# Performance work log

Hardware: AMD Instinct MI355X
Metric: run time of the kernel (lower is better)

## Reference

```python
import jax, jax.numpy as jnp
import numpy as np

V, D, NH, NL, HID = 128000, 512, 8, 2, 1408
HD = D // NH
HALF = HD // 2
B, T, NLAB, LBL = 4, 508, 5, 4
EPS = 1e-5


def setup_inputs() -> dict:
    key = jax.random.key(0)
    ks = jax.random.split(key, 16)
    g = lambda k, sh: (jax.random.normal(k, sh, jnp.float32) * 0.02)
    return {
        "input_ids": jax.random.randint(ks[0], (B, T), 0, V),
        "label_ids": jax.random.randint(ks[1], (NLAB, LBL), 0, V),
        "emb": g(ks[2], (V, D)),
        "wq": g(ks[3], (NL, D, D)),
        "wk": g(ks[4], (NL, D, D)),
        "wv": g(ks[5], (NL, D, D)),
        "wo": g(ks[6], (NL, D, D)),
        "w1": g(ks[7], (NL, D, HID)),
        "w2": g(ks[8], (NL, HID, D)),
        "w3": g(ks[9], (NL, D, HID)),
        "attn_norm_w": jnp.ones((NL, D), jnp.float32),
        "ffn_norm_w": jnp.ones((NL, D), jnp.float32),
        "final_norm_w": jnp.ones((D,), jnp.float32),
        "lm_head": g(ks[10], (D, V)),
    }


def _rmsnorm(x, w):
    return x * jax.lax.rsqrt(jnp.mean(x * x, axis=-1, keepdims=True) + EPS) * w


def _score(input_ids, label_ids, emb, wq, wk, wv, wo, w1, w2, w3,
           attn_norm_w, ffn_norm_w, final_norm_w, lm_head):
    Bc, Tc = input_ids.shape
    nl, Lc = label_ids.shape
    S = Tc + Lc
    # pad_id is None in the original (tokenizer attr missing) -> all lengths == T.
    # Causal attention => one forward over [prefix || label] equals the per-token re-forwards.
    ctx = jnp.concatenate([
        jnp.broadcast_to(input_ids[None], (nl, Bc, Tc)),
        jnp.broadcast_to(label_ids[:, None, :], (nl, Bc, Lc)),
    ], axis=-1).reshape(nl * Bc, S)
    N = nl * Bc

    h = emb[ctx]  # [N, S, D]

    # RoPE tables
    pos = jnp.arange(S, dtype=jnp.float32)
    freqs = 1.0 / (10000.0 ** (jnp.arange(HALF, dtype=jnp.float32) / HALF))
    ang = pos[:, None] * freqs[None, :]  # [S, HALF]
    cos = jnp.cos(ang)[None, :, None, :]
    sin = jnp.sin(ang)[None, :, None, :]

    def rope(x):  # x: [N, S, NH, HD]
        x1, x2 = x[..., :HALF], x[..., HALF:]
        return jnp.concatenate([x1 * cos - x2 * sin, x1 * sin + x2 * cos], axis=-1)

    causal = jnp.tril(jnp.ones((S, S), dtype=bool))
    scale = 1.0 / jnp.sqrt(jnp.float32(HD))

    for l in range(NL):
        xn = _rmsnorm(h, attn_norm_w[l])
        q = rope((xn @ wq[l]).reshape(N, S, NH, HD))
        k = rope((xn @ wk[l]).reshape(N, S, NH, HD))
        v = (xn @ wv[l]).reshape(N, S, NH, HD)
        scores = jnp.einsum('nqhd,nkhd->nhqk', q, k) * scale
        scores = jnp.where(causal, scores, jnp.float32(-1e9))
        p = jax.nn.softmax(scores, axis=-1)
        o = jnp.einsum('nhqk,nkhd->nqhd', p, v).reshape(N, S, D)
        h = h + o @ wo[l]
        xn = _rmsnorm(h, ffn_norm_w[l])
        h = h + (jax.nn.silu(xn @ w1[l]) * (xn @ w3[l])) @ w2[l]

    h = _rmsnorm(h, final_norm_w)
    # Only positions T-1 .. T+L-2 predict label tokens; project only those.
    hs = h[:, Tc - 1:Tc - 1 + Lc, :]                    # [N, L, D]
    lp = jax.nn.log_softmax(hs @ lm_head, axis=-1)      # [N, L, V]
    lp = lp.reshape(nl, Bc, Lc, V)
    idx = jnp.broadcast_to(label_ids[:, None, :, None], (nl, Bc, Lc, 1))
    tok_lp = jnp.take_along_axis(lp, idx, axis=-1)[..., 0]  # [nl, B, L]
    return tok_lp.sum(axis=-1).T.astype(jnp.float32)        # [B, num_labels]


def reference(input_ids, label_ids, emb, wq, wk, wv, wo, w1, w2, w3,
              attn_norm_w, ffn_norm_w, final_norm_w, lm_head):
    return _score(input_ids, label_ids, emb, wq, wk, wv, wo, w1, w2, w3,
                  attn_norm_w, ffn_norm_w, final_norm_w, lm_head)
```

## Files before the change

kernel.cpp:

```cpp
#include <hip/hip_runtime.h>
#include <math.h>

typedef unsigned short u16;
typedef unsigned int u32;

namespace {
constexpr int kV = 128000, kD = 512, kNH = 8, kNL = 2, kHID = 1408;
constexpr int kHD = 64, kB = 4, kT = 508, kNLAB = 5, kLBL = 4;
constexpr int kS = 512;
constexpr int kNSeq = kNLAB * kB;
constexpr int kNS = kNSeq * kS;
constexpr int kQKV = 1536;
constexpr float kEps = 1e-5f;
constexpr int kNChunk = 2000;
constexpr int kPad = 56;
constexpr int kStr = 72;
constexpr int kPL = 3211264;
constexpr int oWQ = 0, oWK = 262144, oWV = 524288, oWO = 786432;
constexpr int oW1 = 1048576, oW3 = 1769472, oW2 = 2490368;
}

typedef __attribute__((ext_vector_type(8))) short bf16x8;
typedef __attribute__((ext_vector_type(4))) float f32x4;

__device__ inline u32 pk2(float lo, float hi) {
  u32 ul = __builtin_bit_cast(u32, lo);
  u32 uh = __builtin_bit_cast(u32, hi);
  ul += 0x7fffu + ((ul >> 16) & 1u);
  uh += 0x7fffu + ((uh >> 16) & 1u);
  return (ul >> 16) | (uh & 0xffff0000u);
}
__device__ inline u16 bf1(float x) {
  u32 u = __builtin_bit_cast(u32, x);
  u += 0x7fffu + ((u >> 16) & 1u);
  return (u16)(u >> 16);
}
__device__ inline float bf2f(u16 u) {
  return __builtin_bit_cast(float, ((u32)u) << 16);
}
__device__ inline void gload16(const void* g, void* l) {
  __builtin_amdgcn_global_load_lds(
      (const __attribute__((address_space(1))) void*)g,
      (__attribute__((address_space(3))) void*)l, 16, 0, 0);
}

__global__ __launch_bounds__(256) void k_wtrans_all(const float* __restrict__ wq,
                                                    const float* __restrict__ wk,
                                                    const float* __restrict__ wv,
                                                    const float* __restrict__ wo,
                                                    const float* __restrict__ w1,
                                                    const float* __restrict__ w3,
                                                    const float* __restrict__ w2,
                                                    u16* __restrict__ wT) {
  int bid = blockIdx.x;
  int l = bid / 3136, r = bid % 3136;
  const float* src; u16* dst; int K, N, gxw, t; float scale = 1.f;
  if (r < 1024) {
    int w = r >> 8; t = r & 255; K = 512; N = 512; gxw = 16;
    src = (w == 0 ? wq : w == 1 ? wk : w == 2 ? wv : wo) + (size_t)l * 262144;
    dst = wT + (size_t)l * kPL + w * 262144;
    if (w == 0) scale = 0.125f;
  } else if (r < 2432) {
    int rr = r - 1024; int w = rr / 704; t = rr - w * 704; K = 512; N = 1408; gxw = 44;
    src = (w ? w3 : w1) + (size_t)l * 720896;
    dst = wT + (size_t)l * kPL + (w ? oW3 : oW1);
  } else {
    t = r - 2432; K = 1408; N = 512; gxw = 16;
    src = w2 + (size_t)l * 720896;
    dst = wT + (size_t)l * kPL + oW2;
  }
  int bn = (t % gxw) * 32, bk = (t / gxw) * 32;
  __shared__ float tb[32][33];
  int tid = threadIdx.x;
  int rr2 = tid >> 3, c4 = (tid & 7) * 4;
  float4 v = *(const float4*)(src + (size_t)(bk + rr2) * N + bn + c4);
  tb[rr2][c4 + 0] = v.x * scale; tb[rr2][c4 + 1] = v.y * scale;
  tb[rr2][c4 + 2] = v.z * scale; tb[rr2][c4 + 3] = v.w * scale;
  __syncthreads();
  uint2 o;
  o.x = pk2(tb[c4 + 0][rr2], tb[c4 + 1][rr2]);
  o.y = pk2(tb[c4 + 2][rr2], tb[c4 + 3][rr2]);
  *(uint2*)&dst[(size_t)(bn + rr2) * K + bk + c4] = o;
}

__global__ void k_embed(const int* __restrict__ input_ids, const int* __restrict__ label_ids,
                        const float* __restrict__ emb, float* __restrict__ h) {
  int row = blockIdx.x;
  int n = row / kS, s = row - n * kS;
  int lab = n / kB, b = n - lab * kB;
  int tok = (s < kT) ? input_ids[b * kT + s] : label_ids[lab * kLBL + (s - kT)];
  const float4* src = (const float4*)(emb + (size_t)tok * kD);
  float4* dst = (float4*)(h + (size_t)row * kD);
  for (int i = threadIdx.x; i < kD / 4; i += blockDim.x) dst[i] = src[i];
}

__global__ __launch_bounds__(256) void k_rmsnorm(const float* __restrict__ x,
                                                 const float* __restrict__ w,
                                                 u16* __restrict__ y) {
  int row = blockIdx.x;
  int tid = threadIdx.x;
  const float* xr = x + (size_t)row * kD;
  int i = tid * 2;
  float v0 = xr[i], v1 = xr[i + 1];
  float ss = v0 * v0 + v1 * v1;
  #pragma unroll
  for (int o = 1; o < 64; o <<= 1) ss += __shfl_xor(ss, o);
  __shared__ float wsum[4];
  int lane = tid & 63, wid = tid >> 6;
  if (lane == 0) wsum[wid] = ss;
  __syncthreads();
  float tot = wsum[0] + wsum[1] + wsum[2] + wsum[3];
  float inv = rsqrtf(tot / (float)kD + kEps);
  *(u32*)&y[(size_t)row * kD + i] = pk2(v0 * inv * w[i], v1 * inv * w[i + 1]);
}

template<int MODE>
__global__ __launch_bounds__(256) void k_gemm_bf16(const u16* __restrict__ A,
                                                   const u16* __restrict__ Bt,
                                                   void* __restrict__ Cv,
                                                   int M, int N, int K, int gx) {
  __shared__ u16 As[4 * 128 * 16];
  __shared__ u16 Bs[4 * 128 * 16];
  int nwg = gridDim.x;
  int q8 = nwg >> 3;
  int wg = (blockIdx.x & 7) * q8 + (blockIdx.x >> 3);
  int by = wg / gx, bx = wg - by * gx;
  int row0 = by * 128, col0 = bx * 128;
  int tid = threadIdx.x;
  int wave = tid >> 6, lane = tid & 63;
  int wm = wave >> 1, wn = wave & 1;
  int l15 = lane & 15, l16 = lane >> 4;
  f32x4 acc[4][4];
  #pragma unroll
  for (int i = 0; i < 4; i++)
    #pragma unroll
    for (int j = 0; j < 4; j++) acc[i][j] = (f32x4){0.f, 0.f, 0.f, 0.f};

  int sR = lane >> 1, sS = (lane & 1) * 8;

  for (int k0 = 0; k0 < K; k0 += 64) {
    #pragma unroll
    for (int i = 0; i < 4; i++) {
      int rr = i * 32 + sR;
      gload16(A + (size_t)(row0 + rr) * K + k0 + wave * 16 + sS,
              (char*)As + (wave * 4 + i) * 1024);
      gload16(Bt + (size_t)(col0 + rr) * K + k0 + wave * 16 + sS,
              (char*)Bs + (wave * 4 + i) * 1024);
    }
    __syncthreads();
    #pragma unroll
    for (int kk = 0; kk < 2; kk++) {
      int qq = kk * 2 + (l16 >> 1);
      int sub = (l16 & 1) * 8;
      bf16x8 af[4], bfr[4];
      #pragma unroll
      for (int mf = 0; mf < 4; mf++)
        af[mf] = *(const bf16x8*)&As[qq * 2048 + (wm * 64 + mf * 16 + l15) * 16 + sub];
      #pragma unroll
      for (int nf = 0; nf < 4; nf++)
        bfr[nf] = *(const bf16x8*)&Bs[qq * 2048 + (wn * 64 + nf * 16 + l15) * 16 + sub];
      #pragma unroll
      for (int mf = 0; mf < 4; mf++)
        #pragma unroll
        for (int nf = 0; nf < 4; nf++)
          acc[mf][nf] = __builtin_amdgcn_mfma_f32_16x16x32_bf16(af[mf], bfr[nf], acc[mf][nf], 0, 0, 0);
    }
    __syncthreads();
  }
  #pragma unroll
  for (int mf = 0; mf < 4; mf++)
    #pragma unroll
    for (int nf = 0; nf < 4; nf++)
      #pragma unroll
      for (int r = 0; r < 4; r++) {
        int row = row0 + wm * 64 + mf * 16 + l16 * 4 + r;
        int col = col0 + wn * 64 + nf * 16 + l15;
        size_t off = (size_t)row * N + col;
        if (MODE == 1) ((float*)Cv)[off] += acc[mf][nf][r];
        else           ((u16*)Cv)[off] = bf1(acc[mf][nf][r]);
      }
}

__global__ __launch_bounds__(256) void k_ffn13_bf16(const u16* __restrict__ A,
                                                    const u16* __restrict__ W1t,
                                                    const u16* __restrict__ W3t,
                                                    u16* __restrict__ act,
                                                    int M, int N, int K, int gx) {
  __shared__ u16 As[4 * 128 * 16];
  __shared__ u16 B1[4 * 128 * 16];
  __shared__ u16 B2[4 * 128 * 16];
  int nwg = gridDim.x;
  int q8 = nwg >> 3;
  int wg = (blockIdx.x & 7) * q8 + (blockIdx.x >> 3);
  int by = wg / gx, bx = wg - by * gx;
  int row0 = by * 128, col0 = bx * 128;
  int tid = threadIdx.x;
  int wave = tid >> 6, lane = tid & 63;
  int wm = wave >> 1, wn = wave & 1;
  int l15 = lane & 15, l16 = lane >> 4;
  f32x4 acc1[4][4], acc2[4][4];
  #pragma unroll
  for (int i = 0; i < 4; i++)
    #pragma unroll
    for (int j = 0; j < 4; j++) {
      acc1[i][j] = (f32x4){0.f, 0.f, 0.f, 0.f};
      acc2[i][j] = (f32x4){0.f, 0.f, 0.f, 0.f};
    }
  int sR = lane >> 1, sS = (lane & 1) * 8;

  for (int k0 = 0; k0 < K; k0 += 64) {
    #pragma unroll
    for (int i = 0; i < 4; i++) {
      int rr = i * 32 + sR;
      gload16(A   + (size_t)(row0 + rr) * K + k0 + wave * 16 + sS,
              (char*)As + (wave * 4 + i) * 1024);
      gload16(W1t + (size_t)(col0 + rr) * K + k0 + wave * 16 + sS,
              (char*)B1 + (wave * 4 + i) * 1024);
      gload16(W3t + (size_t)(col0 + rr) * K + k0 + wave * 16 + sS,
              (char*)B2 + (wave * 4 + i) * 1024);
    }
    __syncthreads();
    #pragma unroll
    for (int kk = 0; kk < 2; kk++) {
      int qq = kk * 2 + (l16 >> 1);
      int sub = (l16 & 1) * 8;
      bf16x8 af[4], b1f[4], b2f[4];
      #pragma unroll
      for (int mf = 0; mf < 4; mf++)
        af[mf] = *(const bf16x8*)&As[qq * 2048 + (wm * 64 + mf * 16 + l15) * 16 + sub];
      #pragma unroll
      for (int nf = 0; nf < 4; nf++) {
        b1f[nf] = *(const bf16x8*)&B1[qq * 2048 + (wn * 64 + nf * 16 + l15) * 16 + sub];
        b2f[nf] = *(const bf16x8*)&B2[qq * 2048 + (wn * 64 + nf * 16 + l15) * 16 + sub];
      }
      #pragma unroll
      for (int mf = 0; mf < 4; mf++)
        #pragma unroll
        for (int nf = 0; nf < 4; nf++) {
          acc1[mf][nf] = __builtin_amdgcn_mfma_f32_16x16x32_bf16(af[mf], b1f[nf], acc1[mf][nf], 0, 0, 0);
          acc2[mf][nf] = __builtin_amdgcn_mfma_f32_16x16x32_bf16(af[mf], b2f[nf], acc2[mf][nf], 0, 0, 0);
        }
    }
    __syncthreads();
  }
  #pragma unroll
  for (int mf = 0; mf < 4; mf++)
    #pragma unroll
    for (int nf = 0; nf < 4; nf++)
      #pragma unroll
      for (int r = 0; r < 4; r++) {
        int row = row0 + wm * 64 + mf * 16 + l16 * 4 + r;
        int col = col0 + wn * 64 + nf * 16 + l15;
        float aa = acc1[mf][nf][r];
        float sg = 1.f / (1.f + expf(-aa));
        act[(size_t)row * N + col] = bf1(aa * sg * acc2[mf][nf][r]);
      }
}

__global__ void k_rope(u16* __restrict__ qkv) {
  int idx = blockIdx.x * blockDim.x + threadIdx.x;
  if (idx >= kNS * kNH * 16) return;
  int d2 = (idx & 15) * 2;
  int t = idx >> 4;
  int hh = t & (kNH - 1);
  int row = t >> 3;
  int s = row & (kS - 1);
  float fa = expf(-0.2878231366242558f * (float)d2);
  float fb = expf(-0.2878231366242558f * (float)(d2 + 1));
  float aa = (float)s * fa, ab = (float)s * fb;
  float ca = cosf(aa), sa = sinf(aa);
  float cb = cosf(ab), sb = sinf(ab);
  size_t base = (size_t)row * kQKV + hh * kHD + d2;
  u32 q1 = *(u32*)&qkv[base], q2 = *(u32*)&qkv[base + 32];
  float x1a = bf2f((u16)q1), x1b = bf2f((u16)(q1 >> 16));
  float x2a = bf2f((u16)q2), x2b = bf2f((u16)(q2 >> 16));
  *(u32*)&qkv[base]      = pk2(x1a * ca - x2a * sa, x1b * cb - x2b * sb);
  *(u32*)&qkv[base + 32] = pk2(x1a * sa + x2a * ca, x1b * sb + x2b * cb);
  u32 k1 = *(u32*)&qkv[base + 512], k2 = *(u32*)&qkv[base + 544];
  x1a = bf2f((u16)k1); x1b = bf2f((u16)(k1 >> 16));
  x2a = bf2f((u16)k2); x2b = bf2f((u16)(k2 >> 16));
  *(u32*)&qkv[base + 512] = pk2(x1a * ca - x2a * sa, x1b * cb - x2b * sb);
  *(u32*)&qkv[base + 544] = pk2(x1a * sa + x2a * ca, x1b * sb + x2b * cb);
}

__global__ __launch_bounds__(256) void k_attn_mfma(const u16* __restrict__ qkv,
                                                   u16* __restrict__ o) {
  int qt = blockIdx.x;
  int nh = blockIdx.y;
  int hh = nh & (kNH - 1), n = nh >> 3;
  int tid = threadIdx.x;
  int wq = tid >> 6, lane = tid & 63;
  int l15 = lane & 15, l16 = lane >> 4;
  __shared__ u16 Ks[64 * kStr];
  __shared__ u16 Vt[64 * kStr];
  __shared__ u16 Ps[4][16 * kStr];
  int q0 = qt * 64;
  int qrow = q0 + wq * 16 + l15;

  bf16x8 qf[2];
  {
    const u16* qg = qkv + (size_t)(n * kS + qrow) * kQKV + hh * kHD;
    qf[0] = *(const bf16x8*)(qg + l16 * 8);
    qf[1] = *(const bf16x8*)(qg + 32 + l16 * 8);
  }

  f32x4 oacc[4];
  #pragma unroll
  for (int i = 0; i < 4; i++) oacc[i] = (f32x4){0.f, 0.f, 0.f, 0.f};
  float m_run = -1e30f, l_run = 0.f;

  int skv = tid & 63, sd0 = (tid >> 6) * 16;

  for (int jt = 0; jt <= qt; jt++) {
    int j0 = jt * 64;
    __syncthreads();
    {
      size_t gb = (size_t)(n * kS + j0 + skv) * kQKV + 512 + hh * kHD + sd0;
      const u16* kg = qkv + gb;
      *(uint4*)&Ks[skv * kStr + sd0]     = *(const uint4*)kg;
      *(uint4*)&Ks[skv * kStr + sd0 + 8] = *(const uint4*)(kg + 8);
      union { uint4 u4[2]; u16 us[16]; } vb;
      vb.u4[0] = *(const uint4*)(kg + 512);
      vb.u4[1] = *(const uint4*)(kg + 520);
      #pragma unroll
      for (int i = 0; i < 16; i++) Vt[(sd0 + i) * kStr + skv] = vb.us[i];
    }
    __syncthreads();

    f32x4 st[4];
    #pragma unroll
    for (int kt = 0; kt < 4; kt++) {
      bf16x8 ka0 = *(const bf16x8*)&Ks[(kt * 16 + l15) * kStr + l16 * 8];
      bf16x8 ka1 = *(const bf16x8*)&Ks[(kt * 16 + l15) * kStr + 32 + l16 * 8];
      f32x4 c = (f32x4){0.f, 0.f, 0.f, 0.f};
      c = __builtin_amdgcn_mfma_f32_16x16x32_bf16(ka0, qf[0], c, 0, 0, 0);
      c = __builtin_amdgcn_mfma_f32_16x16x32_bf16(ka1, qf[1], c, 0, 0, 0);
      st[kt] = c;
    }

    float mx = m_run;
    #pragma unroll
    for (int kt = 0; kt < 4; kt++)
      #pragma unroll
      for (int r = 0; r < 4; r++) {
        int kvg = j0 + kt * 16 + l16 * 4 + r;
        if (kvg > qrow) st[kt][r] = -1e30f;
        mx = fmaxf(mx, st[kt][r]);
      }
    mx = fmaxf(mx, __shfl_xor(mx, 16));
    mx = fmaxf(mx, __shfl_xor(mx, 32));
    float sc = __expf(m_run - mx);
    float p[4][4];
    float rs = 0.f;
    #pragma unroll
    for (int kt = 0; kt < 4; kt++)
      #pragma unroll
      for (int r = 0; r < 4; r++) { p[kt][r] = __expf(st[kt][r] - mx); rs += p[kt][r]; }
    rs += __shfl_xor(rs, 16);
    rs += __shfl_xor(rs, 32);
    l_run = l_run * sc + rs;
    m_run = mx;
    #pragma unroll
    for (int dt = 0; dt < 4; dt++)
      #pragma unroll
      for (int r = 0; r < 4; r++) oacc[dt][r] *= sc;

    #pragma unroll
    for (int kt = 0; kt < 4; kt++) {
      uint2 w2;
      w2.x = pk2(p[kt][0], p[kt][1]);
      w2.y = pk2(p[kt][2], p[kt][3]);
      *(uint2*)&Ps[wq][l15 * kStr + kt * 16 + l16 * 4] = w2;
    }
    asm volatile("s_waitcnt lgkmcnt(0)" ::: "memory");
    __builtin_amdgcn_sched_barrier(0);

    bf16x8 pf0 = *(const bf16x8*)&Ps[wq][l15 * kStr + l16 * 8];
    bf16x8 pf1 = *(const bf16x8*)&Ps[wq][l15 * kStr + 32 + l16 * 8];
    #pragma unroll
    for (int dt = 0; dt < 4; dt++) {
      bf16x8 va0 = *(const bf16x8*)&Vt[(dt * 16 + l15) * kStr + l16 * 8];
      bf16x8 va1 = *(const bf16x8*)&Vt[(dt * 16 + l15) * kStr + 32 + l16 * 8];
      oacc[dt] = __builtin_amdgcn_mfma_f32_16x16x32_bf16(va0, pf0, oacc[dt], 0, 0, 0);
      oacc[dt] = __builtin_amdgcn_mfma_f32_16x16x32_bf16(va1, pf1, oacc[dt], 0, 0, 0);
    }
  }

  float inv = 1.f / l_run;
  u16* og = o + (size_t)(n * kS + qrow) * kD + hh * kHD;
  #pragma unroll
  for (int dt = 0; dt < 4; dt++) {
    uint2 ow;
    ow.x = pk2(oacc[dt][0] * inv, oacc[dt][1] * inv);
    ow.y = pk2(oacc[dt][2] * inv, oacc[dt][3] * inv);
    *(uint2*)(og + dt * 16 + l16 * 4) = ow;
  }
}

__global__ void k_gather(const u16* __restrict__ xn, u16* __restrict__ hs) {
  int r = blockIdx.x;
  int n = r / kLBL, li = r - n * kLBL;
  size_t src = ((size_t)n * kS + (kT - 1 + li)) * kD;
  int i = threadIdx.x;
  *(uint2*)&hs[(size_t)r * kD + i * 4] = *(const uint2*)&xn[src + i * 4];
}

__global__ __launch_bounds__(256) void k_logits_mfma(const u16* __restrict__ hs,
                                                     const float* __restrict__ lm,
                                                     float* __restrict__ part) {
  __shared__ u16 As[80 * kPad];
  __shared__ u16 Bs[256 * kPad];
  int tid = threadIdx.x;
  int wave = tid >> 6, lane = tid & 63;
  int l15 = lane & 15, l16 = lane >> 4;
  int col0 = blockIdx.x * 256;
  f32x4 acc[5][4];
  #pragma unroll
  for (int i = 0; i < 5; i++)
    #pragma unroll
    for (int j = 0; j < 4; j++) acc[i][j] = (f32x4){0.f, 0.f, 0.f, 0.f};

  int arow = tid >> 1, ahalf = tid & 1;
  int bkp = tid >> 4, bf4 = tid & 15;

  for (int k0 = 0; k0 < kD; k0 += 32) {
    if (tid < 160) {
      const u16* ag = hs + (size_t)arow * kD + k0 + ahalf * 16;
      *(uint4*)&As[arow * kPad + ahalf * 16]     = *(const uint4*)ag;
      *(uint4*)&As[arow * kPad + ahalf * 16 + 8] = *(const uint4*)(ag + 8);
    }
    #pragma unroll
    for (int t = 0; t < 4; t++) {
      int colq = bf4 + 16 * t;
      const float* bg = lm + (size_t)(k0 + 2 * bkp) * kV + col0 + colq * 4;
      float4 lo = *(const float4*)bg;
      float4 hi = *(const float4*)(bg + kV);
      *(u32*)&Bs[(colq * 4 + 0) * kPad + 2 * bkp] = pk2(lo.x, hi.x);
      *(u32*)&Bs[(colq * 4 + 1) * kPad + 2 * bkp] = pk2(lo.y, hi.y);
      *(u32*)&Bs[(colq * 4 + 2) * kPad + 2 * bkp] = pk2(lo.z, hi.z);
      *(u32*)&Bs[(colq * 4 + 3) * kPad + 2 * bkp] = pk2(lo.w, hi.w);
    }
    __syncthreads();
    bf16x8 af[5], bfr[4];
    #pragma unroll
    for (int mf = 0; mf < 5; mf++)
      af[mf] = *(const bf16x8*)&As[(mf * 16 + l15) * kPad + l16 * 8];
    #pragma unroll
    for (int nf = 0; nf < 4; nf++)
      bfr[nf] = *(const bf16x8*)&Bs[(wave * 64 + nf * 16 + l15) * kPad + l16 * 8];
    #pragma unroll
    for (int mf = 0; mf < 5; mf++)
      #pragma unroll
      for (int nf = 0; nf < 4; nf++)
        acc[mf][nf] = __builtin_amdgcn_mfma_f32_16x16x32_bf16(af[mf], bfr[nf], acc[mf][nf], 0, 0, 0);
    __syncthreads();
  }

  int chunk = blockIdx.x * 4 + wave;
  #pragma unroll
  for (int mf = 0; mf < 5; mf++)
    #pragma unroll
    for (int r = 0; r < 4; r++) {
      float mx = fmaxf(fmaxf(acc[mf][0][r], acc[mf][1][r]),
                       fmaxf(acc[mf][2][r], acc[mf][3][r]));
      #pragma unroll
      for (int off = 1; off < 16; off <<= 1) mx = fmaxf(mx, __shfl_xor(mx, off));
      float se = expf(acc[mf][0][r] - mx) + expf(acc[mf][1][r] - mx) +
                 expf(acc[mf][2][r] - mx) + expf(acc[mf][3][r] - mx);
      #pragma unroll
      for (int off = 1; off < 16; off <<= 1) se += __shfl_xor(se, off);
      if (l15 == 0) {
        int row = mf * 16 + l16 * 4 + r;
        size_t pi = ((size_t)row * kNChunk + chunk) * 2;
        part[pi] = mx; part[pi + 1] = se;
      }
    }
}

__global__ __launch_bounds__(64) void k_label_logits(const u16* __restrict__ hs,
                                                     const float* __restrict__ lm,
                                                     const int* __restrict__ label_ids,
                                                     float* __restrict__ lbl) {
  int r = blockIdx.x;
  int li = r & 3, n = r >> 2, lab = n / kB;
  int tok = label_ids[lab * kLBL + li];
  int lane = threadIdx.x;
  float dv = 0.f;
  for (int d2 = lane; d2 < kD; d2 += 64)
    dv += bf2f(hs[(size_t)r * kD + d2]) * lm[(size_t)d2 * kV + tok];
  #pragma unroll
  for (int o2 = 1; o2 < 64; o2 <<= 1) dv += __shfl_xor(dv, o2);
  if (lane == 0) lbl[r] = dv;
}

__global__ __launch_bounds__(64) void k_final(const float* __restrict__ part,
                                              const float* __restrict__ lbl,
                                              float* __restrict__ out) {
  int n = blockIdx.x;
  int lab = n / kB, b = n - lab * kB;
  int lane = threadIdx.x;
  float res = 0.f;
  for (int li = 0; li < kLBL; li++) {
    int r = n * kLBL + li;
    const float* pr = part + (size_t)r * kNChunk * 2;
    float mx = -1e30f;
    for (int c = lane; c < kNChunk; c += 64) mx = fmaxf(mx, pr[c * 2]);
    #pragma unroll
    for (int o2 = 1; o2 < 64; o2 <<= 1) mx = fmaxf(mx, __shfl_xor(mx, o2));
    float sum = 0.f;
    for (int c = lane; c < kNChunk; c += 64) sum += pr[c * 2 + 1] * expf(pr[c * 2] - mx);
    #pragma unroll
    for (int o2 = 1; o2 < 64; o2 <<= 1) sum += __shfl_xor(sum, o2);
    res += lbl[r] - (mx + logf(sum));
  }
  if (lane == 0) out[b * kNLAB + lab] = res;
}

extern "C" void kernel_launch(void* const* d_in, const int* in_sizes, int n_in,
                              void* d_out, int out_size, void* d_ws, size_t ws_size,
                              hipStream_t stream) {
  const int*   input_ids    = (const int*)d_in[0];
  const int*   label_ids    = (const int*)d_in[1];
  const float* emb          = (const float*)d_in[2];
  const float* wq           = (const float*)d_in[3];
  const float* wk           = (const float*)d_in[4];
  const float* wv           = (const float*)d_in[5];
  const float* wo           = (const float*)d_in[6];
  const float* w1           = (const float*)d_in[7];
  const float* w2           = (const float*)d_in[8];
  const float* w3           = (const float*)d_in[9];
  const float* attn_norm_w  = (const float*)d_in[10];
  const float* ffn_norm_w   = (const float*)d_in[11];
  const float* final_norm_w = (const float*)d_in[12];
  const float* lm_head      = (const float*)d_in[13];
  float* out = (float*)d_out;

  char* ws = (char*)d_ws;
  float* h    = (float*)(ws);
  u16*   xn   = (u16*)(ws + 20971520);
  u16*   qkv  = (u16*)(ws + 31457280);
  u16*   big  = (u16*)(ws + 62914560);
  u16*   hsb  = (u16*)(ws + 91750400);
  float* part = (float*)(ws + 91832320);
  float* lbl  = (float*)(ws + 93112320);
  u16*   wT   = (u16*)(ws + 93112640);

  k_wtrans_all<<<2 * 3136, 256, 0, stream>>>(wq, wk, wv, wo, w1, w3, w2, wT);
  k_embed<<<kNS, 128, 0, stream>>>(input_ids, label_ids, emb, h);

  for (int l = 0; l < kNL; l++) {
    u16* base = wT + (size_t)l * kPL;
    k_rmsnorm<<<kNS, 256, 0, stream>>>(h, attn_norm_w + (size_t)l * kD, xn);
    k_gemm_bf16<0><<<960, 256, 0, stream>>>(xn, base + oWQ, qkv, kNS, kQKV, kD, 12);
    k_rope<<<(kNS * kNH * 16) / 256, 256, 0, stream>>>(qkv);
    dim3 gattn(kS / 64, kNSeq * kNH);
    k_attn_mfma<<<gattn, 256, 0, stream>>>(qkv, big);
    k_gemm_bf16<1><<<320, 256, 0, stream>>>(big, base + oWO, h, kNS, kD, kD, 4);
    k_rmsnorm<<<kNS, 256, 0, stream>>>(h, ffn_norm_w + (size_t)l * kD, xn);
    k_ffn13_bf16<<<880, 256, 0, stream>>>(xn, base + oW1, base + oW3, big, kNS, kHID, kD, 11);
    k_gemm_bf16<1><<<320, 256, 0, stream>>>(big, base + oW2, h, kNS, kD, kHID, 4);
  }

  k_rmsnorm<<<kNS, 256, 0, stream>>>(h, final_norm_w, xn);
  k_gather<<<kNSeq * kLBL, 128, 0, stream>>>(xn, hsb);
  k_logits_mfma<<<kV / 256, 256, 0, stream>>>(hsb, lm_head, part);
  k_label_logits<<<kNSeq * kLBL, 64, 0, stream>>>(hsb, lm_head, label_ids, lbl);
  k_final<<<kNSeq, 64, 0, stream>>>(part, lbl, out);
}
```

Before: 634.3 us.

## Tile-block operand layouts, fuse RoPE into QKV GEMM, and trim tail kernels

Activations and transposed weights are stored in a 128x64 tiled layout, so each GEMM k-step loads one contiguous 16 KB block with coalesced global-to-LDS loads. RoPE moves into the QKV GEMM epilogue, which removes the separate read-modify-write pass over q and k. The N=512 GEMMs switch to 128x64 tiles, doubling the grid from 320 to 640 blocks for better occupancy. The final rmsnorm now runs only on the 80 gathered rows, and the label-logit dot products are folded into the final reduction kernel. Approximate __sincosf and __expf replace the accurate calls, which adds some numeric error.

```diff
diff --git a/kernel.cpp b/kernel.cpp
--- a/kernel.cpp
+++ b/kernel.cpp
@@ -42,6 +42,10 @@
   __builtin_amdgcn_global_load_lds(
       (const __attribute__((address_space(1))) void*)g,
       (__attribute__((address_space(3))) void*)l, 16, 0, 0);
+}
+__device__ inline size_t tix(int Kt, int row, int k) {
+  return ((size_t)(row >> 7) * Kt + (k >> 6)) * 8192 +
+         ((((k >> 4) & 3) * 2 + ((k >> 3) & 1)) * 128 + (row & 127)) * 8 + (k & 7);
 }
 
 __global__ __launch_bounds__(256) void k_wtrans_all(const float* __restrict__ wq,
@@ -80,7 +84,7 @@
   uint2 o;
   o.x = pk2(tb[c4 + 0][rr2], tb[c4 + 1][rr2]);
   o.y = pk2(tb[c4 + 2][rr2], tb[c4 + 3][rr2]);
-  *(uint2*)&dst[(size_t)(bn + rr2) * K + bk + c4] = o;
+  *(uint2*)&dst[tix(K >> 6, bn + rr2, bk + c4)] = o;
 }
 
 __global__ void k_embed(const int* __restrict__ input_ids, const int* __restrict__ label_ids,
@@ -111,20 +115,16 @@
   __syncthreads();
   float tot = wsum[0] + wsum[1] + wsum[2] + wsum[3];
   float inv = rsqrtf(tot / (float)kD + kEps);
-  *(u32*)&y[(size_t)row * kD + i] = pk2(v0 * inv * w[i], v1 * inv * w[i + 1]);
-}
-
-template<int MODE>
-__global__ __launch_bounds__(256) void k_gemm_bf16(const u16* __restrict__ A,
-                                                   const u16* __restrict__ Bt,
-                                                   void* __restrict__ Cv,
-                                                   int M, int N, int K, int gx) {
-  __shared__ u16 As[4 * 128 * 16];
-  __shared__ u16 Bs[4 * 128 * 16];
-  int nwg = gridDim.x;
-  int q8 = nwg >> 3;
-  int wg = (blockIdx.x & 7) * q8 + (blockIdx.x >> 3);
-  int by = wg / gx, bx = wg - by * gx;
+  *(u32*)&y[tix(8, row, i)] = pk2(v0 * inv * w[i], v1 * inv * w[i + 1]);
+}
+
+__global__ __launch_bounds__(256) void k_gemm_qkv(const u16* __restrict__ A,
+                                                  const u16* __restrict__ Bt,
+                                                  u16* __restrict__ qkv) {
+  __shared__ u16 As[8192];
+  __shared__ u16 Bs[8192];
+  int wg = (blockIdx.x & 7) * 120 + (blockIdx.x >> 3);
+  int by = wg / 12, bx = wg - by * 12;
   int row0 = by * 128, col0 = bx * 128;
   int tid = threadIdx.x;
   int wave = tid >> 6, lane = tid & 63;
@@ -136,29 +136,25 @@
     #pragma unroll
     for (int j = 0; j < 4; j++) acc[i][j] = (f32x4){0.f, 0.f, 0.f, 0.f};
 
-  int sR = lane >> 1, sS = (lane & 1) * 8;
-
-  for (int k0 = 0; k0 < K; k0 += 64) {
+  for (int kt = 0; kt < 8; kt++) {
+    const u16* Ab = A  + ((size_t)(row0 >> 7) * 8 + kt) * 8192;
+    const u16* Bb = Bt + ((size_t)(col0 >> 7) * 8 + kt) * 8192;
     #pragma unroll
     for (int i = 0; i < 4; i++) {
-      int rr = i * 32 + sR;
-      gload16(A + (size_t)(row0 + rr) * K + k0 + wave * 16 + sS,
-              (char*)As + (wave * 4 + i) * 1024);
-      gload16(Bt + (size_t)(col0 + rr) * K + k0 + wave * 16 + sS,
-              (char*)Bs + (wave * 4 + i) * 1024);
-    }
-    __syncthreads();
-    #pragma unroll
-    for (int kk = 0; kk < 2; kk++) {
-      int qq = kk * 2 + (l16 >> 1);
-      int sub = (l16 & 1) * 8;
+      int off = ((wave * 2 + (i >> 1)) * 128 + (i & 1) * 64) * 8;
+      gload16(Ab + off + (size_t)lane * 8, (char*)As + off * 2);
+      gload16(Bb + off + (size_t)lane * 8, (char*)Bs + off * 2);
+    }
+    __syncthreads();
+    #pragma unroll
+    for (int h = 0; h < 2; h++) {
       bf16x8 af[4], bfr[4];
       #pragma unroll
       for (int mf = 0; mf < 4; mf++)
-        af[mf] = *(const bf16x8*)&As[qq * 2048 + (wm * 64 + mf * 16 + l15) * 16 + sub];
+        af[mf] = *(const bf16x8*)&As[((h * 4 + l16) * 128 + wm * 64 + mf * 16 + l15) * 8];
       #pragma unroll
       for (int nf = 0; nf < 4; nf++)
-        bfr[nf] = *(const bf16x8*)&Bs[qq * 2048 + (wn * 64 + nf * 16 + l15) * 16 + sub];
+        bfr[nf] = *(const bf16x8*)&Bs[((h * 4 + l16) * 128 + wn * 64 + nf * 16 + l15) * 8];
       #pragma unroll
       for (int mf = 0; mf < 4; mf++)
         #pragma unroll
@@ -167,32 +163,112 @@
     }
     __syncthreads();
   }
-  #pragma unroll
-  for (int mf = 0; mf < 4; mf++)
+
+  if (bx < 8) {
+    #pragma unroll
+    for (int nf = 0; nf < 2; nf++) {
+      int d = nf * 16 + l15;
+      float fr = __expf(-0.2878231366242558f * (float)d);
+      #pragma unroll
+      for (int mf = 0; mf < 4; mf++)
+        #pragma unroll
+        for (int r = 0; r < 4; r++) {
+          int row = row0 + wm * 64 + mf * 16 + l16 * 4 + r;
+          int s = row & (kS - 1);
+          float sn, cs;
+          __sincosf((float)s * fr, &sn, &cs);
+          float x1 = acc[mf][nf][r], x2 = acc[mf][nf + 2][r];
+          size_t base = (size_t)row * kQKV + col0 + wn * 64 + nf * 16 + l15;
+          qkv[base]      = bf1(x1 * cs - x2 * sn);
+          qkv[base + 32] = bf1(x1 * sn + x2 * cs);
+        }
+    }
+  } else {
+    #pragma unroll
+    for (int mf = 0; mf < 4; mf++)
+      #pragma unroll
+      for (int nf = 0; nf < 4; nf++)
+        #pragma unroll
+        for (int r = 0; r < 4; r++) {
+          int row = row0 + wm * 64 + mf * 16 + l16 * 4 + r;
+          qkv[(size_t)row * kQKV + col0 + wn * 64 + nf * 16 + l15] = bf1(acc[mf][nf][r]);
+        }
+  }
+}
+
+__global__ __launch_bounds__(256) void k_gemm_n64(const u16* __restrict__ A,
+                                                  const u16* __restrict__ Bt,
+                                                  float* __restrict__ C,
+                                                  int Kt, int N) {
+  __shared__ u16 As[8192];
+  __shared__ u16 Bs[4096];
+  int nwg = gridDim.x;
+  int wg = (blockIdx.x & 7) * (nwg >> 3) + (blockIdx.x >> 3);
+  int by = wg >> 3, bx = wg & 7;
+  int row0 = by * 128, col0 = bx * 64;
+  int p = col0 >> 7, half = (col0 >> 6) & 1;
+  int tid = threadIdx.x;
+  int wave = tid >> 6, lane = tid & 63;
+  int l15 = lane & 15, l16 = lane >> 4;
+  f32x4 acc[2][4];
+  #pragma unroll
+  for (int i = 0; i < 2; i++)
+    #pragma unroll
+    for (int j = 0; j < 4; j++) acc[i][j] = (f32x4){0.f, 0.f, 0.f, 0.f};
+
+  for (int kt = 0; kt < Kt; kt++) {
+    const u16* Ab = A  + ((size_t)(row0 >> 7) * Kt + kt) * 8192;
+    const u16* Bb = Bt + ((size_t)p * Kt + kt) * 8192;
+    #pragma unroll
+    for (int i = 0; i < 4; i++) {
+      int off = ((wave * 2 + (i >> 1)) * 128 + (i & 1) * 64) * 8;
+      gload16(Ab + off + (size_t)lane * 8, (char*)As + off * 2);
+    }
+    #pragma unroll
+    for (int sl = 0; sl < 2; sl++) {
+      int ch = wave * 2 + sl;
+      gload16(Bb + (ch * 128 + half * 64) * 8 + (size_t)lane * 8,
+              (char*)Bs + (ch * 64) * 16);
+    }
+    __syncthreads();
+    #pragma unroll
+    for (int h = 0; h < 2; h++) {
+      bf16x8 af[2], bfr[4];
+      #pragma unroll
+      for (int mf = 0; mf < 2; mf++)
+        af[mf] = *(const bf16x8*)&As[((h * 4 + l16) * 128 + wave * 32 + mf * 16 + l15) * 8];
+      #pragma unroll
+      for (int nf = 0; nf < 4; nf++)
+        bfr[nf] = *(const bf16x8*)&Bs[((h * 4 + l16) * 64 + nf * 16 + l15) * 8];
+      #pragma unroll
+      for (int mf = 0; mf < 2; mf++)
+        #pragma unroll
+        for (int nf = 0; nf < 4; nf++)
+          acc[mf][nf] = __builtin_amdgcn_mfma_f32_16x16x32_bf16(af[mf], bfr[nf], acc[mf][nf], 0, 0, 0);
+    }
+    __syncthreads();
+  }
+  #pragma unroll
+  for (int mf = 0; mf < 2; mf++)
     #pragma unroll
     for (int nf = 0; nf < 4; nf++)
       #pragma unroll
       for (int r = 0; r < 4; r++) {
-        int row = row0 + wm * 64 + mf * 16 + l16 * 4 + r;
-        int col = col0 + wn * 64 + nf * 16 + l15;
-        size_t off = (size_t)row * N + col;
-        if (MODE == 1) ((float*)Cv)[off] += acc[mf][nf][r];
-        else           ((u16*)Cv)[off] = bf1(acc[mf][nf][r]);
+        int row = row0 + wave * 32 + mf * 16 + l16 * 4 + r;
+        int col = col0 + nf * 16 + l15;
+        C[(size_t)row * N + col] += acc[mf][nf][r];
       }
 }
 
 __global__ __launch_bounds__(256) void k_ffn13_bf16(const u16* __restrict__ A,
                                                     const u16* __restrict__ W1t,
                                                     const u16* __restrict__ W3t,
-                                                    u16* __restrict__ act,
-                                                    int M, int N, int K, int gx) {
-  __shared__ u16 As[4 * 128 * 16];
-  __shared__ u16 B1[4 * 128 * 16];
-  __shared__ u16 B2[4 * 128 * 16];
-  int nwg = gridDim.x;
-  int q8 = nwg >> 3;
-  int wg = (blockIdx.x & 7) * q8 + (blockIdx.x >> 3);
-  int by = wg / gx, bx = wg - by * gx;
+                                                    u16* __restrict__ act) {
+  __shared__ u16 As[8192];
+  __shared__ u16 B1[8192];
+  __shared__ u16 B2[8192];
+  int wg = (blockIdx.x & 7) * 110 + (blockIdx.x >> 3);
+  int by = wg / 11, bx = wg - by * 11;
   int row0 = by * 128, col0 = bx * 128;
   int tid = threadIdx.x;
   int wave = tid >> 6, lane = tid & 63;
@@ -206,32 +282,29 @@
       acc1[i][j] = (f32x4){0.f, 0.f, 0.f, 0.f};
       acc2[i][j] = (f32x4){0.f, 0.f, 0.f, 0.f};
     }
-  int sR = lane >> 1, sS = (lane & 1) * 8;
-
-  for (int k0 = 0; k0 < K; k0 += 64) {
+
+  for (int kt = 0; kt < 8; kt++) {
+    const u16* Ab  = A   + ((size_t)(row0 >> 7) * 8 + kt) * 8192;
+    const u16* B1b = W1t + ((size_t)(col0 >> 7) * 8 + kt) * 8192;
+    const u16* B3b = W3t + ((size_t)(col0 >> 7) * 8 + kt) * 8192;
     #pragma unroll
     for (int i = 0; i < 4; i++) {
-      int rr = i * 32 + sR;
-      gload16(A   + (size_t)(row0 + rr) * K + k0 + wave * 16 + sS,
-              (char*)As + (wave * 4 + i) * 1024);
-      gload16(W1t + (size_t)(col0 + rr) * K + k0 + wave * 16 + sS,
-              (char*)B1 + (wave * 4 + i) * 1024);
-      gload16(W3t + (size_t)(col0 + rr) * K + k0 + wave * 16 + sS,
-              (char*)B2 + (wave * 4 + i) * 1024);
-    }
-    __syncthreads();
-    #pragma unroll
-    for (int kk = 0; kk < 2; kk++) {
-      int qq = kk * 2 + (l16 >> 1);
-      int sub = (l16 & 1) * 8;
+      int off = ((wave * 2 + (i >> 1)) * 128 + (i & 1) * 64) * 8;
+      gload16(Ab  + off + (size_t)lane * 8, (char*)As + off * 2);
+      gload16(B1b + off + (size_t)lane * 8, (char*)B1 + off * 2);
+      gload16(B3b + off + (size_t)lane * 8, (char*)B2 + off * 2);
+    }
+    __syncthreads();
+    #pragma unroll
+    for (int h = 0; h < 2; h++) {
       bf16x8 af[4], b1f[4], b2f[4];
       #pragma unroll
       for (int mf = 0; mf < 4; mf++)
-        af[mf] = *(const bf16x8*)&As[qq * 2048 + (wm * 64 + mf * 16 + l15) * 16 + sub];
+        af[mf] = *(const bf16x8*)&As[((h * 4 + l16) * 128 + wm * 64 + mf * 16 + l15) * 8];
       #pragma unroll
       for (int nf = 0; nf < 4; nf++) {
-        b1f[nf] = *(const bf16x8*)&B1[qq * 2048 + (wn * 64 + nf * 16 + l15) * 16 + sub];
-        b2f[nf] = *(const bf16x8*)&B2[qq * 2048 + (wn * 64 + nf * 16 + l15) * 16 + sub];
+        b1f[nf] = *(const bf16x8*)&B1[((h * 4 + l16) * 128 + wn * 64 + nf * 16 + l15) * 8];
+        b2f[nf] = *(const bf16x8*)&B2[((h * 4 + l16) * 128 + wn * 64 + nf * 16 + l15) * 8];
       }
       #pragma unroll
       for (int mf = 0; mf < 4; mf++)
@@ -252,35 +325,9 @@
         int row = row0 + wm * 64 + mf * 16 + l16 * 4 + r;
         int col = col0 + wn * 64 + nf * 16 + l15;
         float aa = acc1[mf][nf][r];
-        float sg = 1.f / (1.f + expf(-aa));
-        act[(size_t)row * N + col] = bf1(aa * sg * acc2[mf][nf][r]);
+        float sg = 1.f / (1.f + __expf(-aa));
+        act[tix(22, row, col)] = bf1(aa * sg * acc2[mf][nf][r]);
       }
-}
-
-__global__ void k_rope(u16* __restrict__ qkv) {
-  int idx = blockIdx.x * blockDim.x + threadIdx.x;
-  if (idx >= kNS * kNH * 16) return;
-  int d2 = (idx & 15) * 2;
-  int t = idx >> 4;
-  int hh = t & (kNH - 1);
-  int row = t >> 3;
-  int s = row & (kS - 1);
-  float fa = expf(-0.2878231366242558f * (float)d2);
-  float fb = expf(-0.2878231366242558f * (float)(d2 + 1));
-  float aa = (float)s * fa, ab = (float)s * fb;
-  float ca = cosf(aa), sa = sinf(aa);
-  float cb = cosf(ab), sb = sinf(ab);
-  size_t base = (size_t)row * kQKV + hh * kHD + d2;
-  u32 q1 = *(u32*)&qkv[base], q2 = *(u32*)&qkv[base + 32];
-  float x1a = bf2f((u16)q1), x1b = bf2f((u16)(q1 >> 16));
-  float x2a = bf2f((u16)q2), x2b = bf2f((u16)(q2 >> 16));
-  *(u32*)&qkv[base]      = pk2(x1a * ca - x2a * sa, x1b * cb - x2b * sb);
-  *(u32*)&qkv[base + 32] = pk2(x1a * sa + x2a * ca, x1b * sb + x2b * cb);
-  u32 k1 = *(u32*)&qkv[base + 512], k2 = *(u32*)&qkv[base + 544];
-  x1a = bf2f((u16)k1); x1b = bf2f((u16)(k1 >> 16));
-  x2a = bf2f((u16)k2); x2b = bf2f((u16)(k2 >> 16));
-  *(u32*)&qkv[base + 512] = pk2(x1a * ca - x2a * sa, x1b * cb - x2b * sb);
-  *(u32*)&qkv[base + 544] = pk2(x1a * sa + x2a * ca, x1b * sb + x2b * cb);
 }
 
 __global__ __launch_bounds__(256) void k_attn_mfma(const u16* __restrict__ qkv,
@@ -387,22 +434,38 @@
   }
 
   float inv = 1.f / l_run;
-  u16* og = o + (size_t)(n * kS + qrow) * kD + hh * kHD;
+  int rowIdx = n * kS + qrow;
   #pragma unroll
   for (int dt = 0; dt < 4; dt++) {
     uint2 ow;
     ow.x = pk2(oacc[dt][0] * inv, oacc[dt][1] * inv);
     ow.y = pk2(oacc[dt][2] * inv, oacc[dt][3] * inv);
-    *(uint2*)(og + dt * 16 + l16 * 4) = ow;
-  }
-}
-
-__global__ void k_gather(const u16* __restrict__ xn, u16* __restrict__ hs) {
+    size_t base = ((size_t)(rowIdx >> 7) * 8 + hh) * 8192 +
+                  (size_t)(((dt * 2 + ((l16 >> 1) & 1)) * 128 + (rowIdx & 127)) * 8 + (l16 & 1) * 4);
+    *(uint2*)&o[base] = ow;
+  }
+}
+
+__global__ __launch_bounds__(256) void k_rms_gather(const float* __restrict__ x,
+                                                    const float* __restrict__ w,
+                                                    u16* __restrict__ hs) {
   int r = blockIdx.x;
-  int n = r / kLBL, li = r - n * kLBL;
-  size_t src = ((size_t)n * kS + (kT - 1 + li)) * kD;
-  int i = threadIdx.x;
-  *(uint2*)&hs[(size_t)r * kD + i * 4] = *(const uint2*)&xn[src + i * 4];
+  int n = r >> 2, li = r & 3;
+  int row = n * kS + (kT - 1 + li);
+  int tid = threadIdx.x;
+  const float* xr = x + (size_t)row * kD;
+  int i = tid * 2;
+  float v0 = xr[i], v1 = xr[i + 1];
+  float ss = v0 * v0 + v1 * v1;
+  #pragma unroll
+  for (int o = 1; o < 64; o <<= 1) ss += __shfl_xor(ss, o);
+  __shared__ float wsum[4];
+  int lane = tid & 63, wid = tid >> 6;
+  if (lane == 0) wsum[wid] = ss;
+  __syncthreads();
+  float tot = wsum[0] + wsum[1] + wsum[2] + wsum[3];
+  float inv = rsqrtf(tot / (float)kD + kEps);
+  *(u32*)&hs[(size_t)r * kD + i] = pk2(v0 * inv * w[i], v1 * inv * w[i + 1]);
 }
 
 __global__ __launch_bounds__(256) void k_logits_mfma(const u16* __restrict__ hs,
@@ -477,24 +540,10 @@
     }
 }
 
-__global__ __launch_bounds__(64) void k_label_logits(const u16* __restrict__ hs,
-                                                     const float* __restrict__ lm,
-                                                     const int* __restrict__ label_ids,
-                                                     float* __restrict__ lbl) {
-  int r = blockIdx.x;
-  int li = r & 3, n = r >> 2, lab = n / kB;
-  int tok = label_ids[lab * kLBL + li];
-  int lane = threadIdx.x;
-  float dv = 0.f;
-  for (int d2 = lane; d2 < kD; d2 += 64)
-    dv += bf2f(hs[(size_t)r * kD + d2]) * lm[(size_t)d2 * kV + tok];
-  #pragma unroll
-  for (int o2 = 1; o2 < 64; o2 <<= 1) dv += __shfl_xor(dv, o2);
-  if (lane == 0) lbl[r] = dv;
-}
-
 __global__ __launch_bounds__(64) void k_final(const float* __restrict__ part,
-                                              const float* __restrict__ lbl,
+                                              const u16* __restrict__ hs,
+                                              const float* __restrict__ lm,
+                                              const int* __restrict__ label_ids,
                                               float* __restrict__ out) {
   int n = blockIdx.x;
   int lab = n / kB, b = n - lab * kB;
@@ -502,6 +551,12 @@
   float res = 0.f;
   for (int li = 0; li < kLBL; li++) {
     int r = n * kLBL + li;
+    int tok = label_ids[lab * kLBL + li];
+    float dv = 0.f;
+    for (int d2 = lane; d2 < kD; d2 += 64)
+      dv += bf2f(hs[(size_t)r * kD + d2]) * lm[(size_t)d2 * kV + tok];
+    #pragma unroll
+    for (int o2 = 1; o2 < 64; o2 <<= 1) dv += __shfl_xor(dv, o2);
     const float* pr = part + (size_t)r * kNChunk * 2;
     float mx = -1e30f;
     for (int c = lane; c < kNChunk; c += 64) mx = fmaxf(mx, pr[c * 2]);
@@ -511,7 +566,7 @@
     for (int c = lane; c < kNChunk; c += 64) sum += pr[c * 2 + 1] * expf(pr[c * 2] - mx);
     #pragma unroll
     for (int o2 = 1; o2 < 64; o2 <<= 1) sum += __shfl_xor(sum, o2);
-    res += lbl[r] - (mx + logf(sum));
+    res += dv - (mx + logf(sum));
   }
   if (lane == 0) out[b * kNLAB + lab] = res;
 }
@@ -542,7 +597,6 @@
   u16*   big  = (u16*)(ws + 62914560);
   u16*   hsb  = (u16*)(ws + 91750400);
   float* part = (float*)(ws + 91832320);
-  float* lbl  = (float*)(ws + 93112320);
   u16*   wT   = (u16*)(ws + 93112640);
 
   k_wtrans_all<<<2 * 3136, 256, 0, stream>>>(wq, wk, wv, wo, w1, w3, w2, wT);
@@ -551,19 +605,16 @@
   for (int l = 0; l < kNL; l++) {
     u16* base = wT + (size_t)l * kPL;
     k_rmsnorm<<<kNS, 256, 0, stream>>>(h, attn_norm_w + (size_t)l * kD, xn);
-    k_gemm_bf16<0><<<960, 256, 0, stream>>>(xn, base + oWQ, qkv, kNS, kQKV, kD, 12);
-    k_rope<<<(kNS * kNH * 16) / 256, 256, 0, stream>>>(qkv);
+    k_gemm_qkv<<<960, 256, 0, stream>>>(xn, base + oWQ, qkv);
     dim3 gattn(kS / 64, kNSeq * kNH);
     k_attn_mfma<<<gattn, 256, 0, stream>>>(qkv, big);
-    k_gemm_bf16<1><<<320, 256, 0, stream>>>(big, base + oWO, h, kNS, kD, kD, 4);
+    k_gemm_n64<<<640, 256, 0, stream>>>(big, base + oWO, h, 8, kD);
     k_rmsnorm<<<kNS, 256, 0, stream>>>(h, ffn_norm_w + (size_t)l * kD, xn);
-    k_ffn13_bf16<<<880, 256, 0, stream>>>(xn, base + oW1, base + oW3, big, kNS, kHID, kD, 11);
-    k_gemm_bf16<1><<<320, 256, 0, stream>>>(big, base + oW2, h, kNS, kD, kHID, 4);
-  }
-
-  k_rmsnorm<<<kNS, 256, 0, stream>>>(h, final_norm_w, xn);
-  k_gather<<<kNSeq * kLBL, 128, 0, stream>>>(xn, hsb);
+    k_ffn13_bf16<<<880, 256, 0, stream>>>(xn, base + oW1, base + oW3, big);
+    k_gemm_n64<<<640, 256, 0, stream>>>(big, base + oW2, h, 22, kD);
+  }
+
+  k_rms_gather<<<kNSeq * kLBL, 256, 0, stream>>>(h, final_norm_w, hsb);
   k_logits_mfma<<<kV / 256, 256, 0, stream>>>(hsb, lm_head, part);
-  k_label_logits<<<kNSeq * kLBL, 64, 0, stream>>>(hsb, lm_head, label_ids, lbl);
-  k_final<<<kNSeq, 64, 0, stream>>>(part, lbl, out);
-}
+  k_final<<<kNSeq, 64, 0, stream>>>(part, hsb, lm_head, label_ids, out);
+}
```

Measured after the change: 528.8 us. 1.2x faster.
